# Optimization experiments

Measured on AMD Instinct MI355X. Metric: run time of the kernel, lower is better.

Reference implementation:

```python
import jax, jax.numpy as jnp
import numpy as np


def _generate_planes():
    return jnp.array([[[1, 0, 0], [0, 1, 0], [0, 0, 1]],
                      [[0, 1, 0], [0, 0, 1], [1, 0, 0]],
                      [[0, 0, 1], [1, 0, 0], [0, 1, 0]]], dtype=jnp.float32)


def _grid_sample(image, optical):
    # image: [B, C, IH, IW], optical: [B, H, W, 2] in [-1, 1]
    B, C, IH, IW = image.shape
    _, H, W, _ = optical.shape
    ix = (optical[..., 0] + 1) / 2 * (IW - 1)
    iy = (optical[..., 1] + 1) / 2 * (IH - 1)
    # corner coords are non-differentiable (torch.no_grad in original)
    ix_nw = jax.lax.stop_gradient(jnp.floor(ix))
    iy_nw = jax.lax.stop_gradient(jnp.floor(iy))
    ix_se = ix_nw + 1
    iy_se = iy_nw + 1
    # bilinear weights computed with UNclamped corners (matches original order)
    w_nw = (ix_se - ix) * (iy_se - iy)
    w_ne = (ix - ix_nw) * (iy_se - iy)
    w_sw = (ix_se - ix) * (iy - iy_nw)
    w_se = (ix - ix_nw) * (iy - iy_nw)
    # clamp indices for the gathers
    cx0 = jnp.clip(ix_nw, 0, IW - 1).astype(jnp.int32)
    cy0 = jnp.clip(iy_nw, 0, IH - 1).astype(jnp.int32)
    cx1 = jnp.clip(ix_se, 0, IW - 1).astype(jnp.int32)
    cy1 = jnp.clip(iy_se, 0, IH - 1).astype(jnp.int32)
    flat = image.reshape(B, C, IH * IW)

    def gather(cy, cx):
        idx = (cy * IW + cx).reshape(B, 1, H * W)
        v = jnp.take_along_axis(flat, jnp.broadcast_to(idx, (B, C, H * W)), axis=2)
        return v.reshape(B, C, H, W)

    out = (gather(cy0, cx0) * w_nw[:, None] + gather(cy0, cx1) * w_ne[:, None]
           + gather(cy1, cx0) * w_sw[:, None] + gather(cy1, cx1) * w_se[:, None])
    return out


def _project_onto_planes(planes, coordinates):
    # planes: [P, 3, 3]; coordinates: [N, M, 3]
    N, M, _ = coordinates.shape
    P = planes.shape[0]
    inv_planes = jnp.linalg.inv(planes)  # [P, 3, 3]
    # [N, P, M, 3] @ [P, 3, 3] -> [N, P, M, 3]
    proj = jnp.einsum('nmc,pcd->npmd', coordinates, inv_planes)
    return proj.reshape(N * P, M, 3)[..., :2]


def setup_inputs() -> dict:
    key = jax.random.key(0)
    k1, k2 = jax.random.split(key)
    N, P, C, H, W = 1, 3, 32, 256, 256
    M = 524288
    plane_features = jax.random.normal(k1, (N, P, C, H, W), dtype=jnp.float32)
    coordinates = jax.random.uniform(k2, (N, M, 3), dtype=jnp.float32, minval=-1.0, maxval=1.0)
    return {
        'plane_features': plane_features,
        'coordinates': coordinates,
        'plane_axes': _generate_planes(),
        'box_warp': 2,
    }


def reference(plane_features, coordinates, plane_axes, box_warp):
    N, P, C, H, W = plane_features.shape
    _, M, _ = coordinates.shape
    feats = plane_features.reshape(N * P, C, H, W)
    coords = (2.0 / box_warp) * coordinates
    proj = _project_onto_planes(plane_axes, coords)[:, None]  # [N*P, 1, M, 2]
    sampled = _grid_sample(feats, proj)  # [N*P, C, 1, M]
    out = jnp.transpose(sampled, (0, 3, 2, 1)).reshape(N, P, M, C)
    return out
```

## Files before the change

### kernel.cpp

```cpp
#include <hip/hip_runtime.h>

#define PP 3
#define CC 32
#define HH 256
#define WW 256
#define HWP (HH * WW)


__global__ void tp_invert_planes(const float* __restrict__ axes,
                                 const int* __restrict__ box_warp_bits,
                                 float* __restrict__ inv_out) {
    int t = threadIdx.x;
    if (t >= PP) return;
    int bits = *box_warp_bits;
    float bw;
    if (bits >= 1 && bits <= 100000) bw = (float)bits;
    else                             bw = __int_as_float(bits);
    const float* a = axes + t * 9;
    float a00 = a[0], a01 = a[1], a02 = a[2];
    float a10 = a[3], a11 = a[4], a12 = a[5];
    float a20 = a[6], a21 = a[7], a22 = a[8];
    float det = a00 * (a11 * a22 - a12 * a21)
              - a01 * (a10 * a22 - a12 * a20)
              + a02 * (a10 * a21 - a11 * a20);
    float s = (2.0f / bw) / det;
    float* o = inv_out + t * 9;
    o[0] = (a11 * a22 - a12 * a21) * s;
    o[1] = (a02 * a21 - a01 * a22) * s;
    o[2] = (a01 * a12 - a02 * a11) * s;
    o[3] = (a12 * a20 - a10 * a22) * s;
    o[4] = (a00 * a22 - a02 * a20) * s;
    o[5] = (a02 * a10 - a00 * a12) * s;
    o[6] = (a10 * a21 - a11 * a20) * s;
    o[7] = (a01 * a20 - a00 * a21) * s;
    o[8] = (a00 * a11 - a01 * a10) * s;
}

__global__ void tp_transpose(const float* __restrict__ in,
                             float* __restrict__ out) {
    __shared__ float tile[CC][33];
    const int p   = blockIdx.y;
    const int pb  = blockIdx.x * 32;
    const int tid = threadIdx.x;

    const int j     = tid & 31;
    const int cbase = tid >> 5;
    const float* ip = in + (size_t)p * CC * HWP + pb + j;
#pragma unroll
    for (int it = 0; it < 4; ++it) {
        int c = cbase + it * 8;
        tile[c][j] = ip[(size_t)c * HWP];
    }
    __syncthreads();

    const int c4 = tid & 7;
    const int jj = tid >> 3;
    float4 v;
    v.x = tile[c4 * 4 + 0][jj];
    v.y = tile[c4 * 4 + 1][jj];
    v.z = tile[c4 * 4 + 2][jj];
    v.w = tile[c4 * 4 + 3][jj];
    float4* op = (float4*)out + ((size_t)p * HWP + pb + jj) * 8 + c4;
    *op = v;
}

__global__ __launch_bounds__(256) void tp_sample(
        const float* __restrict__ coords,
        const float4* __restrict__ feat_t,
        const float* __restrict__ invp,
        float4* __restrict__ out,
        int M) {
    const int tid = threadIdx.x;
    const int c4  = tid & 7;
    const int m   = blockIdx.x * 32 + (tid >> 3);
    const int p   = blockIdx.y;
    if (m >= M) return;

    const float cx = coords[3 * m + 0];
    const float cy = coords[3 * m + 1];
    const float cz = coords[3 * m + 2];
    const float* iv = invp + p * 9;
    const float px = cx * iv[0] + cy * iv[3] + cz * iv[6];
    const float py = cx * iv[1] + cy * iv[4] + cz * iv[7];

    const float ix = (px + 1.0f) * 0.5f * (float)(WW - 1);
    const float iy = (py + 1.0f) * 0.5f * (float)(HH - 1);
    const float fx0 = floorf(ix), fy0 = floorf(iy);
    const float fx = ix - fx0, fy = iy - fy0;
    int x0 = (int)fx0, y0 = (int)fy0;
    int x1 = x0 + 1,   y1 = y0 + 1;
    x0 = min(max(x0, 0), WW - 1); x1 = min(max(x1, 0), WW - 1);
    y0 = min(max(y0, 0), HH - 1); y1 = min(max(y1, 0), HH - 1);
    const float w00 = (1.0f - fx) * (1.0f - fy);
    const float w01 = fx * (1.0f - fy);
    const float w10 = (1.0f - fx) * fy;
    const float w11 = fx * fy;

    const size_t base = (size_t)p * HWP * 8 + c4;
    const float4 v00 = feat_t[base + (size_t)(y0 * WW + x0) * 8];
    const float4 v01 = feat_t[base + (size_t)(y0 * WW + x1) * 8];
    const float4 v10 = feat_t[base + (size_t)(y1 * WW + x0) * 8];
    const float4 v11 = feat_t[base + (size_t)(y1 * WW + x1) * 8];

    float4 r;
    r.x = v00.x * w00 + v01.x * w01 + v10.x * w10 + v11.x * w11;
    r.y = v00.y * w00 + v01.y * w01 + v10.y * w10 + v11.y * w11;
    r.z = v00.z * w00 + v01.z * w01 + v10.z * w10 + v11.z * w11;
    r.w = v00.w * w00 + v01.w * w01 + v10.w * w10 + v11.w * w11;

    out[((size_t)p * M + m) * 8 + c4] = r;
}

extern "C" void kernel_launch(void* const* d_in, const int* in_sizes, int n_in,
                              void* d_out, int out_size, void* d_ws, size_t ws_size,
                              hipStream_t stream) {
    const float* feats  = (const float*)d_in[0];
    const float* coords = (const float*)d_in[1];
    const float* axes   = (const float*)d_in[2];
    const int*   bw     = (const int*)d_in[3];
    const int M = in_sizes[1] / 3;

    float* trans = (float*)d_ws;
    float* inv   = trans + (size_t)PP * HWP * CC;

    tp_invert_planes<<<1, 64, 0, stream>>>(axes, bw, inv);
    tp_transpose<<<dim3(HWP / 32, PP), 256, 0, stream>>>(feats, trans);
    tp_sample<<<dim3((M + 31) / 32, PP), 256, 0, stream>>>(
        coords, (const float4*)trans, inv, (float4*)d_out, M);
}
```

Before: 295.1 us.

## Fuse plane inversion into sampler and process all three planes per thread

Removes the separate plane-inversion kernel by having each sampling block invert the 3x3 plane matrices into shared memory itself. Each thread now handles all three planes for one point, so coordinates are read once per block through shared memory rather than once per plane. All twelve gathers are issued before any blending to expose memory-level parallelism. Output is written with nontemporal stores to avoid polluting cache. In exchange there is more register pressure per thread and a third as many blocks, and the transpose kernel is unchanged.

```diff
diff --git a/kernel.cpp b/kernel.cpp
--- a/kernel.cpp
+++ b/kernel.cpp
@@ -6,35 +6,8 @@
 #define WW 256
 #define HWP (HH * WW)
 
+typedef float vfloat4 __attribute__((ext_vector_type(4)));
 
-__global__ void tp_invert_planes(const float* __restrict__ axes,
-                                 const int* __restrict__ box_warp_bits,
-                                 float* __restrict__ inv_out) {
-    int t = threadIdx.x;
-    if (t >= PP) return;
-    int bits = *box_warp_bits;
-    float bw;
-    if (bits >= 1 && bits <= 100000) bw = (float)bits;
-    else                             bw = __int_as_float(bits);
-    const float* a = axes + t * 9;
-    float a00 = a[0], a01 = a[1], a02 = a[2];
-    float a10 = a[3], a11 = a[4], a12 = a[5];
-    float a20 = a[6], a21 = a[7], a22 = a[8];
-    float det = a00 * (a11 * a22 - a12 * a21)
-              - a01 * (a10 * a22 - a12 * a20)
-              + a02 * (a10 * a21 - a11 * a20);
-    float s = (2.0f / bw) / det;
-    float* o = inv_out + t * 9;
-    o[0] = (a11 * a22 - a12 * a21) * s;
-    o[1] = (a02 * a21 - a01 * a22) * s;
-    o[2] = (a01 * a12 - a02 * a11) * s;
-    o[3] = (a12 * a20 - a10 * a22) * s;
-    o[4] = (a00 * a22 - a02 * a20) * s;
-    o[5] = (a02 * a10 - a00 * a12) * s;
-    o[6] = (a10 * a21 - a11 * a20) * s;
-    o[7] = (a01 * a20 - a00 * a21) * s;
-    o[8] = (a00 * a11 - a01 * a10) * s;
-}
 
 __global__ void tp_transpose(const float* __restrict__ in,
                              float* __restrict__ out) {
@@ -55,60 +28,108 @@
 
     const int c4 = tid & 7;
     const int jj = tid >> 3;
-    float4 v;
+    vfloat4 v;
     v.x = tile[c4 * 4 + 0][jj];
     v.y = tile[c4 * 4 + 1][jj];
     v.z = tile[c4 * 4 + 2][jj];
     v.w = tile[c4 * 4 + 3][jj];
-    float4* op = (float4*)out + ((size_t)p * HWP + pb + jj) * 8 + c4;
+    vfloat4* op = (vfloat4*)out + ((size_t)p * HWP + pb + jj) * 8 + c4;
     *op = v;
 }
 
-__global__ __launch_bounds__(256) void tp_sample(
+__global__ __launch_bounds__(256) void tp_sample_fused(
         const float* __restrict__ coords,
-        const float4* __restrict__ feat_t,
-        const float* __restrict__ invp,
-        float4* __restrict__ out,
+        const vfloat4* __restrict__ feat_t,
+        const float* __restrict__ axes,
+        const int* __restrict__ box_warp_bits,
+        vfloat4* __restrict__ out,
         int M) {
+    __shared__ float sc[96];
+    __shared__ float siv[27];
     const int tid = threadIdx.x;
-    const int c4  = tid & 7;
-    const int m   = blockIdx.x * 32 + (tid >> 3);
-    const int p   = blockIdx.y;
+    const int mb  = blockIdx.x * 32;
+
+    if (tid < 96 && mb * 3 + tid < M * 3) sc[tid] = coords[(size_t)mb * 3 + tid];
+    if (tid < PP) {
+        int bits = *box_warp_bits;
+        float bw = (bits >= 1 && bits <= 100000) ? (float)bits
+                                                 : __int_as_float(bits);
+        const float* a = axes + tid * 9;
+        float a00 = a[0], a01 = a[1], a02 = a[2];
+        float a10 = a[3], a11 = a[4], a12 = a[5];
+        float a20 = a[6], a21 = a[7], a22 = a[8];
+        float det = a00 * (a11 * a22 - a12 * a21)
+                  - a01 * (a10 * a22 - a12 * a20)
+                  + a02 * (a10 * a21 - a11 * a20);
+        float s = (2.0f / bw) / det;
+        float* o = siv + tid * 9;
+        o[0] = (a11 * a22 - a12 * a21) * s;
+        o[1] = (a02 * a21 - a01 * a22) * s;
+        o[2] = (a01 * a12 - a02 * a11) * s;
+        o[3] = (a12 * a20 - a10 * a22) * s;
+        o[4] = (a00 * a22 - a02 * a20) * s;
+        o[5] = (a02 * a10 - a00 * a12) * s;
+        o[6] = (a10 * a21 - a11 * a20) * s;
+        o[7] = (a01 * a20 - a00 * a21) * s;
+        o[8] = (a00 * a11 - a01 * a10) * s;
+    }
+    __syncthreads();
+
+    const int c4 = tid & 7;
+    const int ml = tid >> 3;
+    const int m  = mb + ml;
     if (m >= M) return;
 
-    const float cx = coords[3 * m + 0];
-    const float cy = coords[3 * m + 1];
-    const float cz = coords[3 * m + 2];
-    const float* iv = invp + p * 9;
-    const float px = cx * iv[0] + cy * iv[3] + cz * iv[6];
-    const float py = cx * iv[1] + cy * iv[4] + cz * iv[7];
+    const float cx = sc[ml * 3 + 0];
+    const float cy = sc[ml * 3 + 1];
+    const float cz = sc[ml * 3 + 2];
 
-    const float ix = (px + 1.0f) * 0.5f * (float)(WW - 1);
-    const float iy = (py + 1.0f) * 0.5f * (float)(HH - 1);
-    const float fx0 = floorf(ix), fy0 = floorf(iy);
-    const float fx = ix - fx0, fy = iy - fy0;
-    int x0 = (int)fx0, y0 = (int)fy0;
-    int x1 = x0 + 1,   y1 = y0 + 1;
-    x0 = min(max(x0, 0), WW - 1); x1 = min(max(x1, 0), WW - 1);
-    y0 = min(max(y0, 0), HH - 1); y1 = min(max(y1, 0), HH - 1);
-    const float w00 = (1.0f - fx) * (1.0f - fy);
-    const float w01 = fx * (1.0f - fy);
-    const float w10 = (1.0f - fx) * fy;
-    const float w11 = fx * fy;
+    int   off[PP][4];
+    float wt[PP][4];
+#pragma unroll
+    for (int p = 0; p < PP; ++p) {
+        const float* iv = siv + p * 9;
+        const float px = cx * iv[0] + cy * iv[3] + cz * iv[6];
+        const float py = cx * iv[1] + cy * iv[4] + cz * iv[7];
+        const float ix = (px + 1.0f) * 0.5f * (float)(WW - 1);
+        const float iy = (py + 1.0f) * 0.5f * (float)(HH - 1);
+        const float fx0 = floorf(ix), fy0 = floorf(iy);
+        const float fx = ix - fx0, fy = iy - fy0;
+        int x0 = (int)fx0, y0 = (int)fy0;
+        int x1 = x0 + 1,   y1 = y0 + 1;
+        x0 = min(max(x0, 0), WW - 1); x1 = min(max(x1, 0), WW - 1);
+        y0 = min(max(y0, 0), HH - 1); y1 = min(max(y1, 0), HH - 1);
+        wt[p][0] = (1.0f - fx) * (1.0f - fy);
+        wt[p][1] = fx * (1.0f - fy);
+        wt[p][2] = (1.0f - fx) * fy;
+        wt[p][3] = fx * fy;
+        const int pbase = p * (HWP * 8) + c4;
+        off[p][0] = pbase + (y0 * WW + x0) * 8;
+        off[p][1] = pbase + (y0 * WW + x1) * 8;
+        off[p][2] = pbase + (y1 * WW + x0) * 8;
+        off[p][3] = pbase + (y1 * WW + x1) * 8;
+    }
 
-    const size_t base = (size_t)p * HWP * 8 + c4;
-    const float4 v00 = feat_t[base + (size_t)(y0 * WW + x0) * 8];
-    const float4 v01 = feat_t[base + (size_t)(y0 * WW + x1) * 8];
-    const float4 v10 = feat_t[base + (size_t)(y1 * WW + x0) * 8];
-    const float4 v11 = feat_t[base + (size_t)(y1 * WW + x1) * 8];
+    vfloat4 v[PP][4];
+#pragma unroll
+    for (int p = 0; p < PP; ++p)
+#pragma unroll
+        for (int k = 0; k < 4; ++k)
+            v[p][k] = feat_t[off[p][k]];
 
-    float4 r;
-    r.x = v00.x * w00 + v01.x * w01 + v10.x * w10 + v11.x * w11;
-    r.y = v00.y * w00 + v01.y * w01 + v10.y * w10 + v11.y * w11;
-    r.z = v00.z * w00 + v01.z * w01 + v10.z * w10 + v11.z * w11;
-    r.w = v00.w * w00 + v01.w * w01 + v10.w * w10 + v11.w * w11;
-
-    out[((size_t)p * M + m) * 8 + c4] = r;
+#pragma unroll
+    for (int p = 0; p < PP; ++p) {
+        vfloat4 r;
+        r.x = v[p][0].x * wt[p][0] + v[p][1].x * wt[p][1]
+            + v[p][2].x * wt[p][2] + v[p][3].x * wt[p][3];
+        r.y = v[p][0].y * wt[p][0] + v[p][1].y * wt[p][1]
+            + v[p][2].y * wt[p][2] + v[p][3].y * wt[p][3];
+        r.z = v[p][0].z * wt[p][0] + v[p][1].z * wt[p][1]
+            + v[p][2].z * wt[p][2] + v[p][3].z * wt[p][3];
+        r.w = v[p][0].w * wt[p][0] + v[p][1].w * wt[p][1]
+            + v[p][2].w * wt[p][2] + v[p][3].w * wt[p][3];
+        __builtin_nontemporal_store(r, &out[((size_t)p * M + m) * 8 + c4]);
+    }
 }
 
 extern "C" void kernel_launch(void* const* d_in, const int* in_sizes, int n_in,
@@ -121,10 +142,8 @@
     const int M = in_sizes[1] / 3;
 
     float* trans = (float*)d_ws;
-    float* inv   = trans + (size_t)PP * HWP * CC;
 
-    tp_invert_planes<<<1, 64, 0, stream>>>(axes, bw, inv);
     tp_transpose<<<dim3(HWP / 32, PP), 256, 0, stream>>>(feats, trans);
-    tp_sample<<<dim3((M + 31) / 32, PP), 256, 0, stream>>>(
-        coords, (const float4*)trans, inv, (float4*)d_out, M);
+    tp_sample_fused<<<dim3((M + 31) / 32), 256, 0, stream>>>(
+        coords, (const vfloat4*)trans, axes, bw, (vfloat4*)d_out, M);
 }
```

After: 318.4 us. 1.08x slower.
